# Kernel optimization log

Measured on AMD Instinct MI355X. Metric: run time of the kernel, lower is better.

Reference implementation:

```python
import jax, jax.numpy as jnp
import numpy as np

B, T, C, DU, OUT = 16, 2048, 1024, 1024, 512
CIF_THRESHOLD = 1.0


def setup_inputs():
    key = jax.random.key(0)
    k0, k1, k2, k3, k4, k5 = jax.random.split(key, 6)
    encoder_out = jax.random.normal(k0, (B, T, C), dtype=jnp.float32)
    input_lengths = (T // 2 + jax.random.randint(k1, (B,), 0, T // 2)).astype(jnp.int32)
    target_lengths = (200 + jax.random.randint(k2, (B,), 0, 300)).astype(jnp.int32)
    s = 1.0 / np.sqrt(C)
    Wd = jax.random.uniform(k3, (DU, C), jnp.float32, -s, s)
    bd = jnp.zeros((DU,), jnp.float32)
    sp = 1.0 / np.sqrt(DU)
    Wp = jax.random.uniform(k4, (1, DU), jnp.float32, -sp, sp)
    bp = jnp.zeros((1,), jnp.float32)
    Wo = jax.random.uniform(k5, (OUT, C), jnp.float32, -s, s)
    return {"encoder_out": encoder_out, "input_lengths": input_lengths,
            "target_lengths": target_lengths, "Wd": Wd, "bd": bd,
            "Wp": Wp, "bp": bp, "Wo": Wo}


def _cif_forward(encoder_out, input_lengths, target_lengths, Wd, bd, Wp, bp, Wo):
    Bsz, Tlen, Cdim = encoder_out.shape
    pos = jnp.arange(Tlen)
    not_pad = (pos[None, :] < input_lengths[:, None]).astype(encoder_out.dtype)  # [B,T]

    # dense weight production: relu(x Wd^T + bd) -> sigmoid(. Wp^T + bp)
    h = jax.nn.relu(jnp.einsum('btc,dc->btd', encoder_out, Wd) + bd)
    weight = jax.nn.sigmoid(jnp.einsum('btd,od->bto', h, Wp)[..., 0] + bp[0])
    org_weight = weight * not_pad

    # training-time scaling so weights sum to target_lengths
    scale = target_lengths.astype(encoder_out.dtype) / (org_weight.sum(-1) + 1e-8)
    weight = org_weight * scale[:, None]

    padding_start_id = input_lengths  # = not_padding_mask.sum(-1)

    def step(carry, xs):
        acc_w, acc_s = carry                     # [B], [B,C]
        w, e, i = xs                             # [B], [B,C], scalar step idx
        fired = (acc_w + w) >= CIF_THRESHOLD     # [B]
        remained = 1.0 - acc_w
        new_w = jnp.where(fired, w - remained, w + acc_w)
        new_s = jnp.where(fired[:, None], (w - remained)[:, None] * e,
                          acc_s + w[:, None] * e)
        f_s = jnp.where(fired[:, None], acc_s + remained[:, None] * e, 0.0)
        f_s = jnp.where((i > padding_start_id)[:, None], 0.0, f_s)
        return (new_w, new_s), f_s

    init = (jnp.zeros((Bsz,), encoder_out.dtype),
            jnp.zeros((Bsz, Cdim), encoder_out.dtype))
    _, fired_states = jax.lax.scan(
        step, init,
        (weight.T, jnp.transpose(encoder_out, (1, 0, 2)), jnp.arange(Tlen)))
    fired_states = jnp.transpose(fired_states, (1, 0, 2))  # [B,T,C]

    fired_marks = jnp.abs(fired_states).sum(-1) != 0.0     # [B,T]
    # stable-compact fired frames to front; pad to T (upper bound of fired_max_length)
    order = jnp.argsort(jnp.logical_not(fired_marks).astype(jnp.int32), axis=1)
    n_fired = fired_marks.sum(-1)                           # [B]
    valid = pos[None, :] < n_fired[:, None]                 # [B,T]
    cif_outputs = jnp.take_along_axis(fired_states, order[:, :, None], axis=1)
    cif_outputs = cif_outputs * valid[:, :, None].astype(cif_outputs.dtype)

    idx = jnp.where(valid, order, 0).astype(jnp.int32)
    prev = jnp.concatenate([jnp.zeros((Bsz, 1), jnp.int32), idx[:, :-1]], axis=1)
    cif_durations = (idx - prev) * valid.astype(jnp.int32)

    base_mask = (pos[None, :] == 0).astype(jnp.int32)       # [1,0,0,...] fallback
    cif_out_padding_mask = jnp.where((n_fired > 0)[:, None],
                                     valid.astype(jnp.int32), base_mask)
    quantity_out = org_weight.sum(-1)                       # training branch
    cif_outputs = jnp.einsum('btc,oc->bto', cif_outputs, Wo)  # bias-free output proj
    return cif_outputs, cif_out_padding_mask, cif_durations, quantity_out


def reference(encoder_out, input_lengths, target_lengths, Wd, bd, Wp, bp, Wo):
    return _cif_forward(encoder_out, input_lengths, target_lengths,
                        Wd, bd, Wp, bp, Wo)
```

## Files before the change

kernel.cpp:

```cpp
#include <hip/hip_runtime.h>
#include <cstdint>
#include <cstddef>

#define BSZ 16
#define TLEN 2048
#define CDIM 1024
#define OUTDIM 512
#define MAXF 512

typedef _Float16 f16x8 __attribute__((ext_vector_type(8)));
typedef _Float16 f16x4 __attribute__((ext_vector_type(4)));
typedef float f32x16 __attribute__((ext_vector_type(16)));

__device__ __forceinline__ void gl_lds16(const void* g, void* l) {
    __builtin_amdgcn_global_load_lds(
        (const __attribute__((address_space(1))) void*)g,
        (__attribute__((address_space(3))) void*)l, 16, 0, 0);
}

struct h2pair { _Float16 h0, h1; };
__device__ __forceinline__ h2pair split2(float a) {
    h2pair o;
    o.h0 = (_Float16)a;
    float r = a - (float)o.h0;
    o.h1 = (_Float16)(r * 2048.0f);
    return o;
}

__global__ __launch_bounds__(128) void k0_split_tiled(
    const float* __restrict__ src_, _Float16* __restrict__ P0,
    _Float16* __restrict__ P1)
{
    const int rgp = blockIdx.x;
    const int ktl = blockIdx.y;
    const int r = threadIdx.x;
    const float* src = src_ + (size_t)(rgp * 128 + r) * CDIM + ktl * 32;
    float v[32];
#pragma unroll
    for (int j = 0; j < 8; j++) *(float4*)&v[j * 4] = *(const float4*)(src + j * 4);
    const size_t tb = (size_t)(rgp * 32 + ktl) * 4096;
#pragma unroll
    for (int c = 0; c < 4; c++) {
        f16x8 h0, h1;
#pragma unroll
        for (int j = 0; j < 8; j++) {
            h2pair s = split2(v[c * 8 + j]);
            h0[j] = s.h0;
            h1[j] = s.h1;
        }
        *(f16x8*)&P0[tb + (c * 128 + r) * 8] = h0;
        *(f16x8*)&P1[tb + (c * 128 + r) * 8] = h1;
    }
}

__global__ __launch_bounds__(256) void k0c_split_wo(
    const float* __restrict__ Wo, _Float16* __restrict__ W0,
    _Float16* __restrict__ W1)
{
    const int i = (blockIdx.x * 256 + threadIdx.x) * 4;
    float4 v = *(const float4*)(Wo + i);
    f16x4 h0, h1;
    h2pair s0 = split2(v.x); h0[0] = s0.h0; h1[0] = s0.h1;
    h2pair s1 = split2(v.y); h0[1] = s1.h0; h1[1] = s1.h1;
    h2pair s2 = split2(v.z); h0[2] = s2.h0; h1[2] = s2.h1;
    h2pair s3 = split2(v.w); h0[3] = s3.h0; h1[3] = s3.h1;
    *(f16x4*)&W0[i] = h0;
    *(f16x4*)&W1[i] = h1;
}

__global__ __launch_bounds__(512, 4) void k1_weight_gemm(
    const _Float16* __restrict__ E0, const _Float16* __restrict__ E1,
    const _Float16* __restrict__ BT0, const _Float16* __restrict__ BT1,
    const float* __restrict__ bd, const float* __restrict__ Wp,
    float* __restrict__ g)
{
    __shared__ __align__(16) _Float16 lds[32768];

    const int tid = threadIdx.x;
    const int lane = tid & 63;
    const int wv = tid >> 6;
    const int l5 = lane & 31;
    const int hi = lane >> 5;
    const int wm = wv & 1;
    const int wn = wv >> 1;
    const int mtb = wm * 64;
    const int ntb = wn * 32;

    const int bx = blockIdx.x;
    const int xcd = bx & 7;
    const int j = bx >> 3;
    const int rg = xcd * 32 + (j >> 3);
    const int dug = j & 7;
    const long row0 = (long)rg * 128;
    const int du0 = dug * 128;

    const int region = wv >> 1;
    const int halfsel = wv & 1;
    const _Float16* srcbase =
        (region == 0) ? E0 : (region == 1) ? E1 : (region == 2) ? BT0 : BT1;
    const size_t tb = (region < 2) ? (size_t)(rg * 32) * 4096
                                   : (size_t)(dug * 32) * 4096;
    const int ldsreg = region * 4096;
    const int cbase = halfsel * 4;

    f32x16 acc[2], accc[2];
#pragma unroll
    for (int mt = 0; mt < 2; mt++)
#pragma unroll
        for (int r = 0; r < 16; r++) { acc[mt][r] = 0.f; accc[mt][r] = 0.f; }

#pragma unroll
    for (int c = 0; c < 4; c++)
        gl_lds16(srcbase + tb + (cbase + c) * 512 + lane * 8,
                 &lds[ldsreg + (cbase + c) * 512]);
    asm volatile("s_waitcnt vmcnt(0)" ::: "memory");
    __builtin_amdgcn_s_barrier();

    for (int kt = 0; kt < 32; ++kt) {
        const int cur = (kt & 1) * 16384;
        const int nxt = cur ^ 16384;

        if (kt < 31) {
            const size_t tbk = tb + (size_t)(kt + 1) * 4096;
#pragma unroll
            for (int c = 0; c < 4; c++)
                gl_lds16(srcbase + tbk + (cbase + c) * 512 + lane * 8,
                         &lds[nxt + ldsreg + (cbase + c) * 512]);
        }
        asm volatile("" ::: "memory");

#pragma unroll
        for (int p = 0; p < 2; p++) {
            const int cq = p * 2 + hi;
            f16x8 A0[2], A1[2], B0, B1;
#pragma unroll
            for (int mt = 0; mt < 2; mt++) {
                const int row = mtb + mt * 32 + l5;
                A0[mt] = *(const f16x8*)&lds[cur + (cq * 128 + row) * 8];
                A1[mt] = *(const f16x8*)&lds[cur + 4096 + (cq * 128 + row) * 8];
            }
            {
                const int row = ntb + l5;
                B0 = *(const f16x8*)&lds[cur + 8192 + (cq * 128 + row) * 8];
                B1 = *(const f16x8*)&lds[cur + 12288 + (cq * 128 + row) * 8];
            }
            __builtin_amdgcn_s_setprio(1);
#pragma unroll
            for (int mt = 0; mt < 2; mt++) {
                acc[mt] = __builtin_amdgcn_mfma_f32_32x32x16_f16(
                    A0[mt], B0, acc[mt], 0, 0, 0);
                accc[mt] = __builtin_amdgcn_mfma_f32_32x32x16_f16(
                    A0[mt], B1, accc[mt], 0, 0, 0);
                accc[mt] = __builtin_amdgcn_mfma_f32_32x32x16_f16(
                    A1[mt], B0, accc[mt], 0, 0, 0);
            }
            __builtin_amdgcn_s_setprio(0);
        }

        if (kt < 31) {
            asm volatile("s_waitcnt vmcnt(0) lgkmcnt(0)" ::: "memory");
            __builtin_amdgcn_s_barrier();
        }
    }

    const float bdv = bd[du0 + ntb + l5];
    const float wpv = Wp[du0 + ntb + l5];
    float pm[2][16];
#pragma unroll
    for (int mt = 0; mt < 2; mt++)
#pragma unroll
        for (int r = 0; r < 16; r++) {
            float h = acc[mt][r] + 4.8828125e-4f * accc[mt][r] + bdv;
            h = h > 0.f ? h : 0.f;
            float s = wpv * h;
            s += __shfl_xor(s, 1);
            s += __shfl_xor(s, 2);
            s += __shfl_xor(s, 4);
            s += __shfl_xor(s, 8);
            s += __shfl_xor(s, 16);
            pm[mt][r] = s;
        }
    float out = 0.f;
#pragma unroll
    for (int mt = 0; mt < 2; mt++)
#pragma unroll
        for (int r = 0; r < 16; r++)
            if (l5 == mt * 16 + r) out = pm[mt][r];
    const int mt_sel = l5 >> 4;
    const int r_sel = l5 & 15;
    const int row = mtb + mt_sel * 32 + (r_sel & 3) + 8 * (r_sel >> 2) + 4 * hi;
    atomicAdd(&g[row0 + row], out);
}

__global__ __launch_bounds__(256) void k2_scan(
    const float* __restrict__ g, const int* __restrict__ in_len,
    const int* __restrict__ tgt_len, const float* __restrict__ bp,
    float* __restrict__ c_a, float* __restrict__ c_b,
    int* __restrict__ fire_t, int* __restrict__ n_fired,
    float* __restrict__ out_mask, float* __restrict__ out_dur,
    float* __restrict__ out_qty)
{
    __shared__ float w[TLEN];
    __shared__ float ca[TLEN];
    __shared__ float cb[TLEN];
    __shared__ int fires[MAXF];
    __shared__ float ssum[256];
    __shared__ float s_scale;
    __shared__ int s_nf;

    const int b = blockIdx.x;
    const int tid = threadIdx.x;
    const int len = in_len[b];
    const float bpv = bp[0];

    float local = 0.f;
    for (int t = tid; t < TLEN; t += 256) {
        float gv = g[b * TLEN + t] + bpv;
        float s = 1.f / (1.f + expf(-gv));
        float ow = (t < len) ? s : 0.f;
        w[t] = ow;
        local += ow;
    }
    ssum[tid] = local;
    __syncthreads();
    for (int st = 128; st > 0; st >>= 1) {
        if (tid < st) ssum[tid] += ssum[tid + st];
        __syncthreads();
    }
    if (tid == 0) {
        float org_sum = ssum[0];
        out_qty[b] = org_sum;
        s_scale = (float)tgt_len[b] / (org_sum + 1e-8f);
    }
    __syncthreads();
    float scale = s_scale;
    for (int t = tid; t < TLEN; t += 256) w[t] *= scale;
    __syncthreads();

    if (tid == 0) {
        float accw = 0.f;
        int k = 0;
        int t = 0;
        for (; t + 8 <= len; t += 8) {
            float4 wa = *(const float4*)&w[t];
            float4 wb4 = *(const float4*)&w[t + 4];
            float wv8[8] = {wa.x, wa.y, wa.z, wa.w, wb4.x, wb4.y, wb4.z, wb4.w};
#pragma unroll
            for (int u = 0; u < 8; u++) {
                float wt = wv8[u];
                float aw = accw + wt;
                bool f = (aw >= 1.0f);
                float rem = 1.0f - accw;
                float fb = wt - rem;
                ca[t + u] = f ? rem : wt;
                cb[t + u] = f ? fb : 0.f;
                fires[k & (MAXF - 1)] = t + u;
                k += f ? 1 : 0;
                accw = f ? fb : aw;
            }
        }
        for (; t < len; t++) {
            float wt = w[t];
            float aw = accw + wt;
            bool f = (aw >= 1.0f);
            float rem = 1.0f - accw;
            float fb = wt - rem;
            ca[t] = f ? rem : wt;
            cb[t] = f ? fb : 0.f;
            fires[k & (MAXF - 1)] = t;
            k += f ? 1 : 0;
            accw = f ? fb : aw;
        }
        s_nf = (k < MAXF) ? k : MAXF;
        n_fired[b] = s_nf;
    }
    __syncthreads();

    for (int t = tid; t < len; t += 256) {
        c_a[b * TLEN + t] = ca[t];
        c_b[b * TLEN + t] = cb[t];
    }
    const int nf = s_nf;
    for (int jj = tid; jj < nf; jj += 256) {
        int tj = fires[jj];
        fire_t[b * MAXF + jj] = tj;
        out_mask[b * TLEN + jj] = 1.0f;
        int prev = (jj == 0) ? 0 : fires[jj - 1];
        out_dur[b * TLEN + jj] = (float)(tj - prev);
    }
    if (tid == 0 && nf == 0) out_mask[b * TLEN] = 1.0f;
}

__global__ __launch_bounds__(256) void k3a_compact(
    const float* __restrict__ enc, const float* __restrict__ c_a,
    const float* __restrict__ c_b, const int* __restrict__ fire_t,
    const int* __restrict__ n_fired, _Float16* __restrict__ C0,
    _Float16* __restrict__ C1)
{
    const int b = blockIdx.y;
    const int k = blockIdx.x;
    const int tid = threadIdx.x;
    _Float16* d0 = C0 + ((size_t)b * MAXF + k) * CDIM + tid * 4;
    _Float16* d1 = C1 + ((size_t)b * MAXF + k) * CDIM + tid * 4;
    if (k >= n_fired[b]) {
        f16x4 z = {(_Float16)0.f, (_Float16)0.f, (_Float16)0.f, (_Float16)0.f};
        *(f16x4*)d0 = z;
        *(f16x4*)d1 = z;
        return;
    }
    const int tend = fire_t[b * MAXF + k];
    const int tprev = (k == 0) ? -1 : fire_t[b * MAXF + k - 1];
    float ax = 0.f, ay = 0.f, az = 0.f, aw = 0.f;
    const int tstart = (tprev < 0) ? 0 : tprev;
    for (int t = tstart; t <= tend; t++) {
        float coef = (t == tprev) ? c_b[b * TLEN + t] : c_a[b * TLEN + t];
        const float4 e = *(const float4*)(enc + ((size_t)b * TLEN + t) * CDIM + tid * 4);
        ax += coef * e.x;
        ay += coef * e.y;
        az += coef * e.z;
        aw += coef * e.w;
    }
    f16x4 h0, h1;
    h2pair s0 = split2(ax); h0[0] = s0.h0; h1[0] = s0.h1;
    h2pair s1 = split2(ay); h0[1] = s1.h0; h1[1] = s1.h1;
    h2pair s2 = split2(az); h0[2] = s2.h0; h1[2] = s2.h1;
    h2pair s3 = split2(aw); h0[3] = s3.h0; h1[3] = s3.h1;
    *(f16x4*)d0 = h0;
    *(f16x4*)d1 = h1;
}

__global__ __launch_bounds__(256, 2) void k3b_outproj(
    const _Float16* __restrict__ C0, const _Float16* __restrict__ C1,
    const _Float16* __restrict__ W0, const _Float16* __restrict__ W1,
    const int* __restrict__ n_fired, float* __restrict__ out0)
{
    __shared__ __align__(16) _Float16 lds[16384];

    const int b = blockIdx.z;
    const int nf = n_fired[b];
    const int j0 = blockIdx.x * 128;
    if (j0 >= nf) return;
    const int o0 = blockIdx.y * 128;
    const int tid = threadIdx.x;
    const int lane = tid & 63;
    const int wv = tid >> 6;
    const int l5 = lane & 31;
    const int hi = lane >> 5;
    const int mtb = (wv & 1) * 64;
    const int ntb = (wv >> 1) * 64;

    const int sr = tid >> 1;
    const int sh = tid & 1;
    const _Float16* a0p = C0 + ((size_t)b * MAXF + j0 + sr) * CDIM + sh * 16;
    const _Float16* a1p = C1 + ((size_t)b * MAXF + j0 + sr) * CDIM + sh * 16;
    const _Float16* b0p = W0 + (size_t)(o0 + sr) * CDIM + sh * 16;
    const _Float16* b1p = W1 + (size_t)(o0 + sr) * CDIM + sh * 16;

    f32x16 acc[2][2], accc[2][2];
#pragma unroll
    for (int mt = 0; mt < 2; mt++)
#pragma unroll
        for (int nt = 0; nt < 2; nt++)
#pragma unroll
            for (int r = 0; r < 16; r++) { acc[mt][nt][r] = 0.f; accc[mt][nt][r] = 0.f; }

    f16x8 xa0[2], xa1[2], xb0[2], xb1[2];
#pragma unroll
    for (int c = 0; c < 2; c++) {
        xa0[c] = *(const f16x8*)(a0p + c * 8);
        xa1[c] = *(const f16x8*)(a1p + c * 8);
        xb0[c] = *(const f16x8*)(b0p + c * 8);
        xb1[c] = *(const f16x8*)(b1p + c * 8);
    }

    for (int kt = 0; kt < 32; ++kt) {
        __syncthreads();
#pragma unroll
        for (int c = 0; c < 2; c++) {
            *(f16x8*)&lds[((sh * 2 + c) * 128 + sr) * 8] = xa0[c];
            *(f16x8*)&lds[4096 + ((sh * 2 + c) * 128 + sr) * 8] = xa1[c];
            *(f16x8*)&lds[8192 + ((sh * 2 + c) * 128 + sr) * 8] = xb0[c];
            *(f16x8*)&lds[12288 + ((sh * 2 + c) * 128 + sr) * 8] = xb1[c];
        }
        __syncthreads();
        if (kt < 31) {
            const int o = (kt + 1) * 32;
#pragma unroll
            for (int c = 0; c < 2; c++) {
                xa0[c] = *(const f16x8*)(a0p + o + c * 8);
                xa1[c] = *(const f16x8*)(a1p + o + c * 8);
                xb0[c] = *(const f16x8*)(b0p + o + c * 8);
                xb1[c] = *(const f16x8*)(b1p + o + c * 8);
            }
        }
#pragma unroll
        for (int ks = 0; ks < 2; ks++) {
            const int ch = ks * 2 + hi;
            f16x8 A0[2], A1[2], B0[2], B1[2];
#pragma unroll
            for (int mt = 0; mt < 2; mt++) {
                const int row = mtb + mt * 32 + l5;
                A0[mt] = *(const f16x8*)&lds[(ch * 128 + row) * 8];
                A1[mt] = *(const f16x8*)&lds[4096 + (ch * 128 + row) * 8];
            }
#pragma unroll
            for (int nt = 0; nt < 2; nt++) {
                const int row = ntb + nt * 32 + l5;
                B0[nt] = *(const f16x8*)&lds[8192 + (ch * 128 + row) * 8];
                B1[nt] = *(const f16x8*)&lds[12288 + (ch * 128 + row) * 8];
            }
#pragma unroll
            for (int mt = 0; mt < 2; mt++)
#pragma unroll
                for (int nt = 0; nt < 2; nt++) {
                    acc[mt][nt] = __builtin_amdgcn_mfma_f32_32x32x16_f16(
                        A0[mt], B0[nt], acc[mt][nt], 0, 0, 0);
                    accc[mt][nt] = __builtin_amdgcn_mfma_f32_32x32x16_f16(
                        A0[mt], B1[nt], accc[mt][nt], 0, 0, 0);
                    accc[mt][nt] = __builtin_amdgcn_mfma_f32_32x32x16_f16(
                        A1[mt], B0[nt], accc[mt][nt], 0, 0, 0);
                }
        }
    }

#pragma unroll
    for (int mt = 0; mt < 2; mt++)
#pragma unroll
        for (int nt = 0; nt < 2; nt++)
#pragma unroll
            for (int r = 0; r < 16; r++) {
                float val = acc[mt][nt][r] + 4.8828125e-4f * accc[mt][nt][r];
                int m = mtb + mt * 32 + (r & 3) + 8 * (r >> 2) + 4 * hi;
                int col = o0 + ntb + nt * 32 + l5;
                out0[((size_t)b * TLEN + j0 + m) * OUTDIM + col] = val;
            }
}

extern "C" void kernel_launch(void* const* d_in, const int* in_sizes, int n_in,
                              void* d_out, int out_size, void* d_ws, size_t ws_size,
                              hipStream_t stream)
{
    const float* enc = (const float*)d_in[0];
    const int* in_len = (const int*)d_in[1];
    const int* tgt_len = (const int*)d_in[2];
    const float* Wd = (const float*)d_in[3];
    const float* bd = (const float*)d_in[4];
    const float* Wp = (const float*)d_in[5];
    const float* bp = (const float*)d_in[6];
    const float* Wo = (const float*)d_in[7];

    char* ws = (char*)d_ws;
    float* g       = (float*)(ws + 0);
    float* c_a     = (float*)(ws + 131072);
    float* c_b     = (float*)(ws + 262144);
    int* fire_t    = (int*)(ws + 393216);
    int* n_fired   = (int*)(ws + 425984);
    _Float16* WdT0 = (_Float16*)(ws + 458752);
    _Float16* WdT1 = (_Float16*)(ws + 2555904);
    _Float16* Wo0  = (_Float16*)(ws + 4653056);
    _Float16* Wo1  = (_Float16*)(ws + 5701632);
    _Float16* C0   = (_Float16*)(ws + 6750208);
    _Float16* C1   = (_Float16*)(ws + 23527424);
    _Float16* E0   = (_Float16*)(ws + 6750208);
    _Float16* E1   = (_Float16*)(ws + 73859072);

    float* out0 = (float*)d_out;
    float* out_mask = out0 + (size_t)BSZ * TLEN * OUTDIM;
    float* out_dur = out_mask + (size_t)BSZ * TLEN;
    float* out_qty = out_dur + (size_t)BSZ * TLEN;

    (void)hipMemsetAsync(g, 0, 131072, stream);
    (void)hipMemsetAsync(d_out, 0, (size_t)out_size * 4, stream);

    k0_split_tiled<<<dim3(8, 32), 128, 0, stream>>>(Wd, WdT0, WdT1);
    k0_split_tiled<<<dim3(256, 32), 128, 0, stream>>>(enc, E0, E1);
    k0c_split_wo<<<512, 256, 0, stream>>>(Wo, Wo0, Wo1);
    k1_weight_gemm<<<2048, 512, 0, stream>>>(E0, E1, WdT0, WdT1, bd, Wp, g);
    k2_scan<<<BSZ, 256, 0, stream>>>(g, in_len, tgt_len, bp, c_a, c_b,
                                     fire_t, n_fired, out_mask, out_dur, out_qty);
    k3a_compact<<<dim3(MAXF, BSZ), 256, 0, stream>>>(enc, c_a, c_b, fire_t,
                                                     n_fired, C0, C1);
    k3b_outproj<<<dim3(4, 4, BSZ), 256, 0, stream>>>(C0, C1, Wo0, Wo1,
                                                     n_fired, out0);
}
```

Before: 652.6 us.

## Restructure weight GEMM with 256-wide N tiles, register-fed B and 4-stage LDS ring

The hi/lo fp16 split kernel now writes 16-wide K tiles in a new tiled layout. The weight-producing GEMM doubles its N tile to 256 per block, halving the grid. B fragments are loaded straight from global memory into registers and double-buffered, while only A goes through a 4-deep LDS ring driven by explicit vmcnt waits. The aim is less LDS traffic and less A reloading per output and deeper prefetch. The cost is more accumulator registers (occupancy hint lowered to 2) and fragile hand-counted waitcnt values.

```diff
diff --git a/kernel.cpp b/kernel.cpp
--- a/kernel.cpp
+++ b/kernel.cpp
@@ -31,25 +31,29 @@
     const float* __restrict__ src_, _Float16* __restrict__ P0,
     _Float16* __restrict__ P1)
 {
-    const int rgp = blockIdx.x;
-    const int ktl = blockIdx.y;
+    const int rg = blockIdx.x;
+    const int kg = blockIdx.y;
     const int r = threadIdx.x;
-    const float* src = src_ + (size_t)(rgp * 128 + r) * CDIM + ktl * 32;
-    float v[32];
-#pragma unroll
-    for (int j = 0; j < 8; j++) *(float4*)&v[j * 4] = *(const float4*)(src + j * 4);
-    const size_t tb = (size_t)(rgp * 32 + ktl) * 4096;
-#pragma unroll
-    for (int c = 0; c < 4; c++) {
-        f16x8 h0, h1;
-#pragma unroll
-        for (int j = 0; j < 8; j++) {
-            h2pair s = split2(v[c * 8 + j]);
-            h0[j] = s.h0;
-            h1[j] = s.h1;
-        }
-        *(f16x8*)&P0[tb + (c * 128 + r) * 8] = h0;
-        *(f16x8*)&P1[tb + (c * 128 + r) * 8] = h1;
+    const float* srow = src_ + (size_t)(rg * 128 + r) * CDIM;
+#pragma unroll
+    for (int i = 0; i < 8; i++) {
+        const int kt = kg * 8 + i;
+#pragma unroll
+        for (int hi = 0; hi < 2; hi++) {
+            float v[8];
+            *(float4*)&v[0] = *(const float4*)(srow + kt * 16 + hi * 8);
+            *(float4*)&v[4] = *(const float4*)(srow + kt * 16 + hi * 8 + 4);
+            f16x8 h0, h1;
+#pragma unroll
+            for (int jj = 0; jj < 8; jj++) {
+                h2pair s = split2(v[jj]);
+                h0[jj] = s.h0;
+                h1[jj] = s.h1;
+            }
+            const size_t o = (size_t)(rg * 64 + kt) * 2048 + (hi * 128 + r) * 8;
+            *(f16x8*)&P0[o] = h0;
+            *(f16x8*)&P1[o] = h1;
+        }
     }
 }
 
@@ -68,13 +72,13 @@
     *(f16x4*)&W1[i] = h1;
 }
 
-__global__ __launch_bounds__(512, 4) void k1_weight_gemm(
+__global__ __launch_bounds__(512, 2) void k1_weight_gemm(
     const _Float16* __restrict__ E0, const _Float16* __restrict__ E1,
     const _Float16* __restrict__ BT0, const _Float16* __restrict__ BT1,
     const float* __restrict__ bd, const float* __restrict__ Wp,
     float* __restrict__ g)
 {
-    __shared__ __align__(16) _Float16 lds[32768];
+    __shared__ __align__(16) _Float16 lds[16384];
 
     const int tid = threadIdx.x;
     const int lane = tid & 63;
@@ -84,108 +88,131 @@
     const int wm = wv & 1;
     const int wn = wv >> 1;
     const int mtb = wm * 64;
-    const int ntb = wn * 32;
 
     const int bx = blockIdx.x;
     const int xcd = bx & 7;
     const int j = bx >> 3;
-    const int rg = xcd * 32 + (j >> 3);
-    const int dug = j & 7;
+    const int rg = xcd * 32 + (j >> 2);
+    const int dug = j & 3;
     const long row0 = (long)rg * 128;
-    const int du0 = dug * 128;
-
-    const int region = wv >> 1;
-    const int halfsel = wv & 1;
-    const _Float16* srcbase =
-        (region == 0) ? E0 : (region == 1) ? E1 : (region == 2) ? BT0 : BT1;
-    const size_t tb = (region < 2) ? (size_t)(rg * 32) * 4096
-                                   : (size_t)(dug * 32) * 4096;
-    const int ldsreg = region * 4096;
-    const int cbase = halfsel * 4;
-
-    f32x16 acc[2], accc[2];
+    const int du0 = dug * 256;
+
+    const int spl = wv >> 2;
+    const int sch = wv & 3;
+    const _Float16* asrc = (spl ? E1 : E0)
+        + (size_t)rg * 64 * 2048 + sch * 512 + lane * 8;
+    const int ldst = spl * 2048 + sch * 512;
+
+    const size_t boff = (size_t)(dug * 2 + (wn >> 1)) * 64 * 2048
+                      + (size_t)(hi * 128 + (wn & 1) * 64 + l5) * 8;
+    const _Float16* bp0 = BT0 + boff;
+    const _Float16* bp1 = BT1 + boff;
+
+    f32x16 acc[2][2], accc[2][2];
 #pragma unroll
     for (int mt = 0; mt < 2; mt++)
 #pragma unroll
-        for (int r = 0; r < 16; r++) { acc[mt][r] = 0.f; accc[mt][r] = 0.f; }
-
-#pragma unroll
-    for (int c = 0; c < 4; c++)
-        gl_lds16(srcbase + tb + (cbase + c) * 512 + lane * 8,
-                 &lds[ldsreg + (cbase + c) * 512]);
-    asm volatile("s_waitcnt vmcnt(0)" ::: "memory");
-    __builtin_amdgcn_s_barrier();
-
-    for (int kt = 0; kt < 32; ++kt) {
-        const int cur = (kt & 1) * 16384;
-        const int nxt = cur ^ 16384;
-
-        if (kt < 31) {
-            const size_t tbk = tb + (size_t)(kt + 1) * 4096;
-#pragma unroll
-            for (int c = 0; c < 4; c++)
-                gl_lds16(srcbase + tbk + (cbase + c) * 512 + lane * 8,
-                         &lds[nxt + ldsreg + (cbase + c) * 512]);
-        }
-        asm volatile("" ::: "memory");
-
-#pragma unroll
-        for (int p = 0; p < 2; p++) {
-            const int cq = p * 2 + hi;
-            f16x8 A0[2], A1[2], B0, B1;
-#pragma unroll
-            for (int mt = 0; mt < 2; mt++) {
-                const int row = mtb + mt * 32 + l5;
-                A0[mt] = *(const f16x8*)&lds[cur + (cq * 128 + row) * 8];
-                A1[mt] = *(const f16x8*)&lds[cur + 4096 + (cq * 128 + row) * 8];
-            }
-            {
-                const int row = ntb + l5;
-                B0 = *(const f16x8*)&lds[cur + 8192 + (cq * 128 + row) * 8];
-                B1 = *(const f16x8*)&lds[cur + 12288 + (cq * 128 + row) * 8];
-            }
-            __builtin_amdgcn_s_setprio(1);
-#pragma unroll
-            for (int mt = 0; mt < 2; mt++) {
-                acc[mt] = __builtin_amdgcn_mfma_f32_32x32x16_f16(
-                    A0[mt], B0, acc[mt], 0, 0, 0);
-                accc[mt] = __builtin_amdgcn_mfma_f32_32x32x16_f16(
-                    A0[mt], B1, accc[mt], 0, 0, 0);
-                accc[mt] = __builtin_amdgcn_mfma_f32_32x32x16_f16(
-                    A1[mt], B0, accc[mt], 0, 0, 0);
-            }
-            __builtin_amdgcn_s_setprio(0);
-        }
-
-        if (kt < 31) {
-            asm volatile("s_waitcnt vmcnt(0) lgkmcnt(0)" ::: "memory");
-            __builtin_amdgcn_s_barrier();
-        }
-    }
-
-    const float bdv = bd[du0 + ntb + l5];
-    const float wpv = Wp[du0 + ntb + l5];
-    float pm[2][16];
+        for (int nt = 0; nt < 2; nt++)
+#pragma unroll
+            for (int r = 0; r < 16; r++) { acc[mt][nt][r] = 0.f; accc[mt][nt][r] = 0.f; }
+
+    f16x8 Bc0[2], Bc1[2], Bn0[2], Bn1[2];
+
+    gl_lds16(asrc + (size_t)0 * 2048, &lds[0 * 4096 + ldst]);
+    asm volatile("" ::: "memory");
+    gl_lds16(asrc + (size_t)1 * 2048, &lds[1 * 4096 + ldst]);
+    asm volatile("" ::: "memory");
+    gl_lds16(asrc + (size_t)2 * 2048, &lds[2 * 4096 + ldst]);
+    asm volatile("" ::: "memory");
+    Bc0[0] = *(const f16x8*)(bp0 + 0);
+    Bc0[1] = *(const f16x8*)(bp0 + 256);
+    Bc1[0] = *(const f16x8*)(bp1 + 0);
+    Bc1[1] = *(const f16x8*)(bp1 + 256);
+
+#define K1_STEP(KT, BC0, BC1, BN0, BN1)                                        \
+    {                                                                          \
+        const int kt_ = (KT);                                                  \
+        __builtin_amdgcn_s_barrier();                                          \
+        __builtin_amdgcn_sched_barrier(0);                                     \
+        if (kt_ <= 60)                                                         \
+            gl_lds16(asrc + (size_t)(kt_ + 3) * 2048,                          \
+                     &lds[((kt_ + 3) & 3) * 4096 + ldst]);                     \
+        asm volatile("" ::: "memory");                                         \
+        if (kt_ <= 62) {                                                       \
+            const size_t bo = (size_t)(kt_ + 1) * 2048;                        \
+            BN0[0] = *(const f16x8*)(bp0 + bo);                                \
+            BN0[1] = *(const f16x8*)(bp0 + bo + 256);                          \
+            BN1[0] = *(const f16x8*)(bp1 + bo);                                \
+            BN1[1] = *(const f16x8*)(bp1 + bo + 256);                          \
+        }                                                                      \
+        if (kt_ == 0)       asm volatile("s_waitcnt vmcnt(11)" ::: "memory");  \
+        else if (kt_ == 1)  asm volatile("s_waitcnt vmcnt(15)" ::: "memory");  \
+        else if (kt_ <= 61) asm volatile("s_waitcnt vmcnt(19)" ::: "memory");  \
+        else if (kt_ == 62) asm volatile("s_waitcnt vmcnt(17)" ::: "memory");  \
+        else                asm volatile("s_waitcnt vmcnt(12)" ::: "memory");  \
+        __builtin_amdgcn_sched_barrier(0);                                     \
+        const int cb = (kt_ & 3) * 4096;                                       \
+        f16x8 A0[2], A1[2];                                                    \
+        _Pragma("unroll")                                                      \
+        for (int mt = 0; mt < 2; mt++) {                                       \
+            const int ro = (hi * 128 + mtb + mt * 32 + l5) * 8;                \
+            A0[mt] = *(const f16x8*)&lds[cb + ro];                             \
+            A1[mt] = *(const f16x8*)&lds[cb + 2048 + ro];                      \
+        }                                                                      \
+        __builtin_amdgcn_s_setprio(1);                                         \
+        _Pragma("unroll")                                                      \
+        for (int mt = 0; mt < 2; mt++)                                         \
+            _Pragma("unroll")                                                  \
+            for (int nt = 0; nt < 2; nt++)                                     \
+                acc[mt][nt] = __builtin_amdgcn_mfma_f32_32x32x16_f16(          \
+                    A0[mt], BC0[nt], acc[mt][nt], 0, 0, 0);                    \
+        _Pragma("unroll")                                                      \
+        for (int mt = 0; mt < 2; mt++)                                         \
+            _Pragma("unroll")                                                  \
+            for (int nt = 0; nt < 2; nt++)                                     \
+                accc[mt][nt] = __builtin_amdgcn_mfma_f32_32x32x16_f16(         \
+                    A0[mt], BC1[nt], accc[mt][nt], 0, 0, 0);                   \
+        _Pragma("unroll")                                                      \
+        for (int mt = 0; mt < 2; mt++)                                         \
+            _Pragma("unroll")                                                  \
+            for (int nt = 0; nt < 2; nt++)                                     \
+                accc[mt][nt] = __builtin_amdgcn_mfma_f32_32x32x16_f16(         \
+                    A1[mt], BC0[nt], accc[mt][nt], 0, 0, 0);                   \
+        __builtin_amdgcn_s_setprio(0);                                         \
+    }
+
+    for (int k2 = 0; k2 < 32; k2++) {
+        K1_STEP(2 * k2,     Bc0, Bc1, Bn0, Bn1);
+        K1_STEP(2 * k2 + 1, Bn0, Bn1, Bc0, Bc1);
+    }
+#undef K1_STEP
+
+    float bdv[2], wpv[2];
+#pragma unroll
+    for (int nt = 0; nt < 2; nt++) {
+        const int n = du0 + wn * 64 + nt * 32 + l5;
+        bdv[nt] = bd[n];
+        wpv[nt] = Wp[n];
+    }
+    float out = 0.f;
 #pragma unroll
     for (int mt = 0; mt < 2; mt++)
 #pragma unroll
         for (int r = 0; r < 16; r++) {
-            float h = acc[mt][r] + 4.8828125e-4f * accc[mt][r] + bdv;
-            h = h > 0.f ? h : 0.f;
-            float s = wpv * h;
+            float s = 0.f;
+#pragma unroll
+            for (int nt = 0; nt < 2; nt++) {
+                float h = acc[mt][nt][r] + 4.8828125e-4f * accc[mt][nt][r] + bdv[nt];
+                h = h > 0.f ? h : 0.f;
+                s += wpv[nt] * h;
+            }
             s += __shfl_xor(s, 1);
             s += __shfl_xor(s, 2);
             s += __shfl_xor(s, 4);
             s += __shfl_xor(s, 8);
             s += __shfl_xor(s, 16);
-            pm[mt][r] = s;
-        }
-    float out = 0.f;
-#pragma unroll
-    for (int mt = 0; mt < 2; mt++)
-#pragma unroll
-        for (int r = 0; r < 16; r++)
-            if (l5 == mt * 16 + r) out = pm[mt][r];
+            if (l5 == mt * 16 + r) out = s;
+        }
     const int mt_sel = l5 >> 4;
     const int r_sel = l5 & 15;
     const int row = mtb + mt_sel * 32 + (r_sel & 3) + 8 * (r_sel >> 2) + 4 * hi;
@@ -472,10 +499,10 @@
     (void)hipMemsetAsync(g, 0, 131072, stream);
     (void)hipMemsetAsync(d_out, 0, (size_t)out_size * 4, stream);
 
-    k0_split_tiled<<<dim3(8, 32), 128, 0, stream>>>(Wd, WdT0, WdT1);
-    k0_split_tiled<<<dim3(256, 32), 128, 0, stream>>>(enc, E0, E1);
+    k0_split_tiled<<<dim3(8, 8), 128, 0, stream>>>(Wd, WdT0, WdT1);
+    k0_split_tiled<<<dim3(256, 8), 128, 0, stream>>>(enc, E0, E1);
     k0c_split_wo<<<512, 256, 0, stream>>>(Wo, Wo0, Wo1);
-    k1_weight_gemm<<<2048, 512, 0, stream>>>(E0, E1, WdT0, WdT1, bd, Wp, g);
+    k1_weight_gemm<<<1024, 512, 0, stream>>>(E0, E1, WdT0, WdT1, bd, Wp, g);
     k2_scan<<<BSZ, 256, 0, stream>>>(g, in_len, tgt_len, bp, c_a, c_b,
                                      fire_t, n_fired, out_mask, out_dur, out_qty);
     k3a_compact<<<dim3(MAXF, BSZ), 256, 0, stream>>>(enc, c_a, c_b, fire_t,
```

New measurement: 664.4 us. Within noise of the previous version (+1.8%).

## Fuse encoder fp16 split into weight GEMM with register-staged prefetch

Applied to the files above, without the earlier changes.

Removes the standalone kernel that split the encoder activations into hi/lo fp16 planes. The weight GEMM now loads fp32 encoder rows into registers one k-tile ahead, splits them in-kernel and writes the result to LDS, while Wd tiles still use direct global-to-LDS loads. This avoids writing and re-reading the large intermediate fp16 buffers. In exchange, each GEMM block re-reads fp32 activations for every DU tile group, and the split arithmetic is added inside the main loop.

```diff
diff --git a/kernel.cpp b/kernel.cpp
--- a/kernel.cpp
+++ b/kernel.cpp
@@ -27,18 +27,18 @@
     return o;
 }
 
-__global__ __launch_bounds__(128) void k0_split_tiled(
-    const float* __restrict__ src_, _Float16* __restrict__ P0,
-    _Float16* __restrict__ P1)
-{
-    const int rgp = blockIdx.x;
+__global__ __launch_bounds__(128) void k0a_split_wd(
+    const float* __restrict__ Wd, _Float16* __restrict__ B0,
+    _Float16* __restrict__ B1)
+{
+    const int dut = blockIdx.x;
     const int ktl = blockIdx.y;
     const int r = threadIdx.x;
-    const float* src = src_ + (size_t)(rgp * 128 + r) * CDIM + ktl * 32;
+    const float* src = Wd + (size_t)(dut * 128 + r) * CDIM + ktl * 32;
     float v[32];
 #pragma unroll
     for (int j = 0; j < 8; j++) *(float4*)&v[j * 4] = *(const float4*)(src + j * 4);
-    const size_t tb = (size_t)(rgp * 32 + ktl) * 4096;
+    const size_t tb = (size_t)(dut * 32 + ktl) * 4096;
 #pragma unroll
     for (int c = 0; c < 4; c++) {
         f16x8 h0, h1;
@@ -48,8 +48,8 @@
             h0[j] = s.h0;
             h1[j] = s.h1;
         }
-        *(f16x8*)&P0[tb + (c * 128 + r) * 8] = h0;
-        *(f16x8*)&P1[tb + (c * 128 + r) * 8] = h1;
+        *(f16x8*)&B0[tb + (c * 128 + r) * 8] = h0;
+        *(f16x8*)&B1[tb + (c * 128 + r) * 8] = h1;
     }
 }
 
@@ -69,10 +69,9 @@
 }
 
 __global__ __launch_bounds__(512, 4) void k1_weight_gemm(
-    const _Float16* __restrict__ E0, const _Float16* __restrict__ E1,
-    const _Float16* __restrict__ BT0, const _Float16* __restrict__ BT1,
-    const float* __restrict__ bd, const float* __restrict__ Wp,
-    float* __restrict__ g)
+    const float* __restrict__ enc, const _Float16* __restrict__ BT0,
+    const _Float16* __restrict__ BT1, const float* __restrict__ bd,
+    const float* __restrict__ Wp, float* __restrict__ g)
 {
     __shared__ __align__(16) _Float16 lds[32768];
 
@@ -81,10 +80,8 @@
     const int wv = tid >> 6;
     const int l5 = lane & 31;
     const int hi = lane >> 5;
-    const int wm = wv & 1;
-    const int wn = wv >> 1;
-    const int mtb = wm * 64;
-    const int ntb = wn * 32;
+    const int mtb = (wv & 1) * 64;
+    const int ntb = (wv >> 1) * 32;
 
     const int bx = blockIdx.x;
     const int xcd = bx & 7;
@@ -94,14 +91,15 @@
     const long row0 = (long)rg * 128;
     const int du0 = dug * 128;
 
-    const int region = wv >> 1;
-    const int halfsel = wv & 1;
-    const _Float16* srcbase =
-        (region == 0) ? E0 : (region == 1) ? E1 : (region == 2) ? BT0 : BT1;
-    const size_t tb = (region < 2) ? (size_t)(rg * 32) * 4096
-                                   : (size_t)(dug * 32) * 4096;
-    const int ldsreg = region * 4096;
-    const int cbase = halfsel * 4;
+    const int sgrp = wv >> 2;
+    const int sq = wv & 3;
+    const int sr = sgrp * 64 + lane;
+    const float* aptr = enc + (row0 + sr) * (long)CDIM + sq * 8;
+    const int aw0 = (sq * 128 + sr) * 8;
+
+    const _Float16* bsrc = (sgrp ? BT1 : BT0)
+        + (size_t)(dug * 32) * 4096 + sq * 1024 + lane * 8;
+    const int bldofs = 8192 + sgrp * 4096 + sq * 1024;
 
     f32x16 acc[2], accc[2];
 #pragma unroll
@@ -109,25 +107,54 @@
 #pragma unroll
         for (int r = 0; r < 16; r++) { acc[mt][r] = 0.f; accc[mt][r] = 0.f; }
 
-#pragma unroll
-    for (int c = 0; c < 4; c++)
-        gl_lds16(srcbase + tb + (cbase + c) * 512 + lane * 8,
-                 &lds[ldsreg + (cbase + c) * 512]);
-    asm volatile("s_waitcnt vmcnt(0)" ::: "memory");
+    float fa[8];
+
+    *(float4*)&fa[0] = *(const float4*)(aptr + 0);
+    *(float4*)&fa[4] = *(const float4*)(aptr + 4);
+    gl_lds16(bsrc, &lds[bldofs]);
+    gl_lds16(bsrc + 512, &lds[bldofs + 512]);
+    asm volatile("" ::: "memory");
+    {
+        f16x8 h0, h1;
+#pragma unroll
+        for (int jj = 0; jj < 8; jj++) {
+            h2pair s = split2(fa[jj]);
+            h0[jj] = s.h0;
+            h1[jj] = s.h1;
+        }
+        *(f16x8*)&lds[aw0] = h0;
+        *(f16x8*)&lds[4096 + aw0] = h1;
+    }
+    *(float4*)&fa[0] = *(const float4*)(aptr + 32);
+    *(float4*)&fa[4] = *(const float4*)(aptr + 36);
+    asm volatile("s_waitcnt vmcnt(2) lgkmcnt(0)" ::: "memory");
     __builtin_amdgcn_s_barrier();
 
     for (int kt = 0; kt < 32; ++kt) {
         const int cur = (kt & 1) * 16384;
         const int nxt = cur ^ 16384;
+        __builtin_amdgcn_sched_barrier(0);
 
         if (kt < 31) {
-            const size_t tbk = tb + (size_t)(kt + 1) * 4096;
-#pragma unroll
-            for (int c = 0; c < 4; c++)
-                gl_lds16(srcbase + tbk + (cbase + c) * 512 + lane * 8,
-                         &lds[nxt + ldsreg + (cbase + c) * 512]);
-        }
-        asm volatile("" ::: "memory");
+            const _Float16* bs = bsrc + (size_t)(kt + 1) * 4096;
+            gl_lds16(bs, &lds[nxt + bldofs]);
+            gl_lds16(bs + 512, &lds[nxt + bldofs + 512]);
+            asm volatile("" ::: "memory");
+            f16x8 h0, h1;
+#pragma unroll
+            for (int jj = 0; jj < 8; jj++) {
+                h2pair s = split2(fa[jj]);
+                h0[jj] = s.h0;
+                h1[jj] = s.h1;
+            }
+            *(f16x8*)&lds[nxt + aw0] = h0;
+            *(f16x8*)&lds[nxt + 4096 + aw0] = h1;
+            if (kt < 30) {
+                *(float4*)&fa[0] = *(const float4*)(aptr + (kt + 2) * 32);
+                *(float4*)&fa[4] = *(const float4*)(aptr + (kt + 2) * 32 + 4);
+            }
+            asm volatile("" ::: "memory");
+        }
 
 #pragma unroll
         for (int p = 0; p < 2; p++) {
@@ -135,14 +162,14 @@
             f16x8 A0[2], A1[2], B0, B1;
 #pragma unroll
             for (int mt = 0; mt < 2; mt++) {
-                const int row = mtb + mt * 32 + l5;
-                A0[mt] = *(const f16x8*)&lds[cur + (cq * 128 + row) * 8];
-                A1[mt] = *(const f16x8*)&lds[cur + 4096 + (cq * 128 + row) * 8];
+                const int ro = (cq * 128 + mtb + mt * 32 + l5) * 8;
+                A0[mt] = *(const f16x8*)&lds[cur + ro];
+                A1[mt] = *(const f16x8*)&lds[cur + 4096 + ro];
             }
             {
-                const int row = ntb + l5;
-                B0 = *(const f16x8*)&lds[cur + 8192 + (cq * 128 + row) * 8];
-                B1 = *(const f16x8*)&lds[cur + 12288 + (cq * 128 + row) * 8];
+                const int ro = (cq * 128 + ntb + l5) * 8;
+                B0 = *(const f16x8*)&lds[cur + 8192 + ro];
+                B1 = *(const f16x8*)&lds[cur + 12288 + ro];
             }
             __builtin_amdgcn_s_setprio(1);
 #pragma unroll
@@ -158,14 +185,17 @@
         }
 
         if (kt < 31) {
-            asm volatile("s_waitcnt vmcnt(0) lgkmcnt(0)" ::: "memory");
+            if (kt < 30)
+                asm volatile("s_waitcnt vmcnt(2) lgkmcnt(0)" ::: "memory");
+            else
+                asm volatile("s_waitcnt vmcnt(0) lgkmcnt(0)" ::: "memory");
             __builtin_amdgcn_s_barrier();
         }
     }
 
     const float bdv = bd[du0 + ntb + l5];
     const float wpv = Wp[du0 + ntb + l5];
-    float pm[2][16];
+    float out = 0.f;
 #pragma unroll
     for (int mt = 0; mt < 2; mt++)
 #pragma unroll
@@ -178,14 +208,8 @@
             s += __shfl_xor(s, 4);
             s += __shfl_xor(s, 8);
             s += __shfl_xor(s, 16);
-            pm[mt][r] = s;
-        }
-    float out = 0.f;
-#pragma unroll
-    for (int mt = 0; mt < 2; mt++)
-#pragma unroll
-        for (int r = 0; r < 16; r++)
-            if (l5 == mt * 16 + r) out = pm[mt][r];
+            if (l5 == mt * 16 + r) out = s;
+        }
     const int mt_sel = l5 >> 4;
     const int r_sel = l5 & 15;
     const int row = mtb + mt_sel * 32 + (r_sel & 3) + 8 * (r_sel >> 2) + 4 * hi;
@@ -461,8 +485,6 @@
     _Float16* Wo1  = (_Float16*)(ws + 5701632);
     _Float16* C0   = (_Float16*)(ws + 6750208);
     _Float16* C1   = (_Float16*)(ws + 23527424);
-    _Float16* E0   = (_Float16*)(ws + 6750208);
-    _Float16* E1   = (_Float16*)(ws + 73859072);
 
     float* out0 = (float*)d_out;
     float* out_mask = out0 + (size_t)BSZ * TLEN * OUTDIM;
@@ -472,10 +494,9 @@
     (void)hipMemsetAsync(g, 0, 131072, stream);
     (void)hipMemsetAsync(d_out, 0, (size_t)out_size * 4, stream);
 
-    k0_split_tiled<<<dim3(8, 32), 128, 0, stream>>>(Wd, WdT0, WdT1);
-    k0_split_tiled<<<dim3(256, 32), 128, 0, stream>>>(enc, E0, E1);
+    k0a_split_wd<<<dim3(8, 32), 128, 0, stream>>>(Wd, WdT0, WdT1);
     k0c_split_wo<<<512, 256, 0, stream>>>(Wo, Wo0, Wo1);
-    k1_weight_gemm<<<2048, 512, 0, stream>>>(E0, E1, WdT0, WdT1, bd, Wp, g);
+    k1_weight_gemm<<<2048, 512, 0, stream>>>(enc, WdT0, WdT1, bd, Wp, g);
     k2_scan<<<BSZ, 256, 0, stream>>>(g, in_len, tgt_len, bp, c_a, c_b,
                                      fire_t, n_fired, out_mask, out_dur, out_qty);
     k3a_compact<<<dim3(MAXF, BSZ), 256, 0, stream>>>(enc, c_a, c_b, fire_t,
```

Measured after the change: 598.3 us. 8.3% less time.
